# Kernel tuning notes

Measured on AMD Instinct MI355X. Metric: run time of the kernel, lower is better.

The kernel has to match this reference:

```python
import jax, jax.numpy as jnp
import numpy as np

C, N, E = 16, 10000, 40000
OP_DIM, LAY_DIM = 4, 4
NODE_FEAT, CFG_FEAT = 140, 18
GRAPH_IN, GRAPH_OUT, HID = 256, 256, 256
HIDDEN_CH = [256, 256, 256]
N_CONVS = len(HIDDEN_CH) + 1  # 4


def setup_inputs() -> dict:
    key = jax.random.key(0)
    ks = iter(jax.random.split(key, 32))
    inp = {}
    inp['x_node_cfg'] = jax.random.randint(next(ks), (C, N, CFG_FEAT), 0, 8)
    inp['x_feat'] = jax.random.normal(next(ks), (N, NODE_FEAT), dtype=jnp.float32)
    inp['x_op'] = jax.random.randint(next(ks), (N,), 0, 120)
    inp['edge_index'] = jax.random.randint(next(ks), (2, E), 0, N)
    s = 0.05
    inp['emb_op'] = jax.random.normal(next(ks), (120, OP_DIM), dtype=jnp.float32)
    inp['emb_layout'] = jax.random.normal(next(ks), (8, LAY_DIM), dtype=jnp.float32)
    in_dim = OP_DIM + NODE_FEAT + CFG_FEAT * LAY_DIM  # 216
    inp['lin_w'] = jax.random.normal(next(ks), (in_dim, GRAPH_IN), dtype=jnp.float32) * s
    inp['lin_b'] = jnp.zeros((GRAPH_IN,), dtype=jnp.float32)
    # all conv dims are 256 -> stack
    inp['conv_wl'] = jax.random.normal(next(ks), (N_CONVS, GRAPH_IN, GRAPH_IN), dtype=jnp.float32) * s
    inp['conv_bl'] = jnp.zeros((N_CONVS, GRAPH_IN), dtype=jnp.float32)
    inp['conv_wr'] = jax.random.normal(next(ks), (N_CONVS, GRAPH_IN, GRAPH_IN), dtype=jnp.float32) * s
    inp['w1'] = jax.random.normal(next(ks), (GRAPH_OUT, HID), dtype=jnp.float32) * s
    inp['b1'] = jnp.zeros((HID,), dtype=jnp.float32)
    inp['w2'] = jax.random.normal(next(ks), (HID, HID), dtype=jnp.float32) * s
    inp['b2'] = jnp.zeros((HID,), dtype=jnp.float32)
    inp['w3'] = jax.random.normal(next(ks), (HID, 1), dtype=jnp.float32) * s
    inp['b3'] = jnp.zeros((1,), dtype=jnp.float32)
    return inp


def reference(x_node_cfg, x_feat, x_op, edge_index, emb_op, emb_layout,
              lin_w, lin_b, conv_wl, conv_bl, conv_wr, w1, b1, w2, b2, w3, b3):
    c, n = x_node_cfg.shape[0], x_node_cfg.shape[1]
    # feature build: layout-config embedding [C,N,18*4], repeated node feat, op embedding
    cfg = emb_layout[x_node_cfg].reshape(c, n, -1)                    # [C,N,72]
    feat = jnp.broadcast_to(x_feat[None], (c, n, x_feat.shape[1]))    # [C,N,140]
    op = jnp.broadcast_to(emb_op[x_op][None], (c, n, emb_op.shape[1]))# [C,N,4]
    x = jnp.concatenate([feat, cfg, op], axis=2)                      # [C,N,216]
    x = x @ lin_w + lin_b                                             # [C,N,256]

    src, dst = edge_index[0], edge_index[1]
    deg = jnp.zeros((n,), x.dtype).at[dst].add(1.0)
    inv_deg = 1.0 / jnp.maximum(deg, 1.0)                             # scatter-mean denom
    for i in range(conv_wl.shape[0]):
        # SAGEConv: out = lin_l(mean_{j in N(i)} x_j) + lin_r(x_i)
        agg = jnp.zeros_like(x).at[:, dst, :].add(x[:, src, :])
        agg = agg * inv_deg[None, :, None]
        x = jax.nn.relu(agg @ conv_wl[i] + conv_bl[i] + x @ conv_wr[i])

    g = x.mean(axis=1)                                                # [C,256] mean pool
    h = jax.nn.relu(g @ w1 + b1)
    h = jax.nn.relu(h @ w2 + b2)
    out = h @ w3 + b3                                                 # [C,1]
    return out.reshape(-1)
```

## Files before the change

### kernel.cpp

```cpp
#include <hip/hip_runtime.h>

#define N_NODES 10000
#define N_CFG   16
#define N_EDGES 40000
#define UW      512

typedef __attribute__((ext_vector_type(8))) short bf16x8;
typedef __attribute__((ext_vector_type(4))) float floatx4;

__device__ __forceinline__ unsigned short f2bf(float f) {
    union { float f; unsigned int u; } v; v.f = f;
    unsigned int r = (v.u + 0x7fffu + ((v.u >> 16) & 1u)) >> 16;
    return (unsigned short)r;
}
__device__ __forceinline__ float bf2f(unsigned short h) {
    union { unsigned int u; float f; } v; v.u = ((unsigned int)h) << 16;
    return v.f;
}
__device__ __forceinline__ void add8(float* acc, uint4 v) {
    acc[0] += bf2f(v.x & 0xffff); acc[1] += bf2f(v.x >> 16);
    acc[2] += bf2f(v.y & 0xffff); acc[3] += bf2f(v.y >> 16);
    acc[4] += bf2f(v.z & 0xffff); acc[5] += bf2f(v.z >> 16);
    acc[6] += bf2f(v.w & 0xffff); acc[7] += bf2f(v.w >> 16);
}

__device__ __forceinline__ void gl_lds16(const unsigned short* g, unsigned short* l) {
    __builtin_amdgcn_global_load_lds(
        (const __attribute__((address_space(1))) unsigned int*)g,
        (__attribute__((address_space(3))) unsigned int*)l, 16, 0, 0);
}


__global__ __launch_bounds__(256) void k_table(const float* __restrict__ emb_layout,
                                               const float* __restrict__ lin_w,
                                               unsigned short* __restrict__ T) {
    int b = blockIdx.x;
    int j = b >> 3, v = b & 7;
    int d = threadIdx.x;
    float s = 0.f;
#pragma unroll
    for (int t = 0; t < 4; ++t)
        s = fmaf(emb_layout[v * 4 + t], lin_w[(140 + 4 * j + t) * 256 + d], s);
    T[b * 256 + d] = f2bf(s);
}

__global__ __launch_bounds__(256) void k_base(const float* __restrict__ x_feat,
                                              const int* __restrict__ x_op,
                                              const float* __restrict__ emb_op,
                                              const float* __restrict__ lin_w,
                                              const float* __restrict__ lin_b,
                                              unsigned short* __restrict__ base) {
    __shared__ float xf[20][144];
    const int tid = threadIdx.x;
    const int n0 = blockIdx.x * 20;
    for (int j = tid; j < 20 * 140; j += 256)
        xf[j / 140][j % 140] = x_feat[(n0 + j / 140) * 140 + (j % 140)];
    if (tid < 80) {
        int i = tid >> 2, t = tid & 3;
        xf[i][140 + t] = emb_op[x_op[n0 + i] * 4 + t];
    }
    __syncthreads();
    const int d = tid;
    float acc[20];
#pragma unroll
    for (int i = 0; i < 20; ++i) acc[i] = 0.f;
    for (int k = 0; k < 140; ++k) {
        float w = lin_w[k * 256 + d];
#pragma unroll
        for (int i = 0; i < 20; ++i) acc[i] = fmaf(xf[i][k], w, acc[i]);
    }
#pragma unroll
    for (int t = 0; t < 4; ++t) {
        float w = lin_w[(212 + t) * 256 + d];
#pragma unroll
        for (int i = 0; i < 20; ++i) acc[i] = fmaf(xf[i][140 + t], w, acc[i]);
    }
    float bb = lin_b[d];
#pragma unroll
    for (int i = 0; i < 20; ++i)
        base[(n0 + i) * 256 + d] = f2bf(acc[i] + bb);
}

template <int CH>
__global__ __launch_bounds__(256) void k_x0(const unsigned short* __restrict__ base,
                                            const unsigned short* __restrict__ T,
                                            const int* __restrict__ cfg,
                                            unsigned short* __restrict__ U,
                                            int cc) {
    __shared__ int idx[8][18];
    const int tid = threadIdx.x;
    const int n0 = blockIdx.x * 8;
    const int cy = blockIdx.y;
    const int cg = cc * CH + cy;
    if (tid < 144) {
        int nl = tid / 18, j = tid % 18;
        idx[nl][j] = cfg[((size_t)cg * N_NODES + n0 + nl) * 18 + j];
    }
    __syncthreads();
    const int nl = tid >> 5;
    const int colg = (tid & 31) * 8;
    const int n = n0 + nl;
    float acc[8];
    uint4 bv = *(const uint4*)(base + n * 256 + colg);
    acc[0] = bf2f(bv.x & 0xffff); acc[1] = bf2f(bv.x >> 16);
    acc[2] = bf2f(bv.y & 0xffff); acc[3] = bf2f(bv.y >> 16);
    acc[4] = bf2f(bv.z & 0xffff); acc[5] = bf2f(bv.z >> 16);
    acc[6] = bf2f(bv.w & 0xffff); acc[7] = bf2f(bv.w >> 16);
#pragma unroll
    for (int j = 0; j < 18; ++j) {
        uint4 tv = *(const uint4*)(T + (j * 8 + idx[nl][j]) * 256 + colg);
        add8(acc, tv);
    }
    uint4 o;
    o.x = (unsigned int)f2bf(acc[0]) | ((unsigned int)f2bf(acc[1]) << 16);
    o.y = (unsigned int)f2bf(acc[2]) | ((unsigned int)f2bf(acc[3]) << 16);
    o.z = (unsigned int)f2bf(acc[4]) | ((unsigned int)f2bf(acc[5]) << 16);
    o.w = (unsigned int)f2bf(acc[6]) | ((unsigned int)f2bf(acc[7]) << 16);
    *(uint4*)(U + ((size_t)cy * N_NODES + n) * UW + 256 + colg) = o;
}


__global__ void k_deg(const int* __restrict__ ei, int* __restrict__ deg) {
    int e = blockIdx.x * 256 + threadIdx.x;
    if (e < N_EDGES) atomicAdd(&deg[ei[N_EDGES + e]], 1);
}

__global__ __launch_bounds__(256) void k_scan(const int* __restrict__ deg,
                                              int* __restrict__ coff,
                                              float* __restrict__ invd) {
    __shared__ int part[257];
    int t = threadIdx.x;
    const int CHk = 40;
    int start = t * CHk;
    int s = 0;
    for (int i = 0; i < CHk; ++i) {
        int idx = start + i;
        if (idx < N_NODES) s += deg[idx];
    }
    part[t + 1] = s;
    if (t == 0) part[0] = 0;
    __syncthreads();
    if (t == 0)
        for (int i = 1; i <= 256; ++i) part[i] += part[i - 1];
    __syncthreads();
    int run = part[t];
    for (int i = 0; i < CHk; ++i) {
        int idx = start + i;
        if (idx < N_NODES) {
            int d = deg[idx];
            coff[idx] = run; run += d;
            invd[idx] = 1.0f / fmaxf((float)d, 1.0f);
        }
    }
    if (t == 0) coff[N_NODES] = part[256];
}

__global__ void k_fill(const int* __restrict__ ei, const int* __restrict__ coff,
                       int* __restrict__ cur, int* __restrict__ csrc) {
    int e = blockIdx.x * 256 + threadIdx.x;
    if (e < N_EDGES) {
        int d = ei[N_EDGES + e];
        int s = ei[e];
        int pos = atomicAdd(&cur[d], 1);
        csrc[coff[d] + pos] = s;
    }
}

__global__ void k_wsplit(const float* __restrict__ wl, const float* __restrict__ wr,
                         unsigned short* __restrict__ WT) {
    int t = blockIdx.x * 256 + threadIdx.x;
    int i = t >> 17;
    int r = (t >> 8) & 511;
    int nn = t & 255;
    float w = (r < 256) ? wl[i * 65536 + r * 256 + nn]
                        : wr[i * 65536 + (r - 256) * 256 + nn];
    unsigned short hi = f2bf(w);
    unsigned short lo = f2bf(w - bf2f(hi));
    size_t b = (size_t)i * 262144 + (size_t)nn * 1024;
    WT[b + r] = hi;
    WT[b + 512 + r] = lo;
}


__global__ __launch_bounds__(256) void k_agg(unsigned short* __restrict__ U,
                                             const int* __restrict__ coff,
                                             const int* __restrict__ csrc,
                                             const float* __restrict__ invd) {
    const int wave = threadIdx.x >> 6, lane = threadIdx.x & 63;
    const int n = blockIdx.x * 4 + wave;
    const size_t cbase = (size_t)blockIdx.y * 4 * N_NODES;
    const int e0 = coff[n], e1 = coff[n + 1];
    const int h = lane >> 5;
    const int cg = (lane & 31) * 8;
    float acc[4][8];
#pragma unroll
    for (int cy = 0; cy < 4; ++cy)
#pragma unroll
        for (int j = 0; j < 8; ++j) acc[cy][j] = 0.f;
    for (int e = e0 + h; e < e1; e += 2) {
        int s = csrc[e];
        const unsigned short* p = U + (cbase + s) * UW + 256 + cg;
#pragma unroll
        for (int cy = 0; cy < 4; ++cy) {
            uint4 v = *(const uint4*)(p + (size_t)cy * N_NODES * UW);
            add8(acc[cy], v);
        }
    }
#pragma unroll
    for (int cy = 0; cy < 4; ++cy)
#pragma unroll
        for (int j = 0; j < 8; ++j)
            acc[cy][j] += __shfl_xor(acc[cy][j], 32, 64);
    if (h == 0) {
        float iv = invd[n];
#pragma unroll
        for (int cy = 0; cy < 4; ++cy) {
            uint4 o;
            o.x = (unsigned int)f2bf(acc[cy][0] * iv) |
                  ((unsigned int)f2bf(acc[cy][1] * iv) << 16);
            o.y = (unsigned int)f2bf(acc[cy][2] * iv) |
                  ((unsigned int)f2bf(acc[cy][3] * iv) << 16);
            o.z = (unsigned int)f2bf(acc[cy][4] * iv) |
                  ((unsigned int)f2bf(acc[cy][5] * iv) << 16);
            o.w = (unsigned int)f2bf(acc[cy][6] * iv) |
                  ((unsigned int)f2bf(acc[cy][7] * iv) << 16);
            *(uint4*)(U + (cbase + (size_t)cy * N_NODES + n) * UW + cg) = o;
        }
    }
}


__global__ __launch_bounds__(512) void k_gemm(unsigned short* __restrict__ U,
                                              const unsigned short* __restrict__ WTl,
                                              const float* __restrict__ bias) {
    __shared__ unsigned short Asm[128 * 32];
    __shared__ unsigned short Bh[256 * 32];
    __shared__ unsigned short Bl[256 * 32];
    const int tid = threadIdx.x;
    const int lane = tid & 63;
    const int wave = tid >> 6;
    const int wm = wave >> 2;
    const int wn = wave & 3;
    const size_t r0 = (size_t)blockIdx.x * 128;

    const int srow = tid >> 2;
    const int gc = (tid & 3) ^ ((srow >> 1) & 3);

    const int colg = lane & 15, kg = lane >> 4, quad = lane >> 4;
    int aoff[4], boff[4];
#pragma unroll
    for (int t = 0; t < 4; ++t) {
        int ar = wm * 64 + t * 16 + colg;
        aoff[t] = ar * 32 + ((kg ^ ((ar >> 1) & 3)) << 3);
        int br = wn * 64 + t * 16 + colg;
        boff[t] = br * 32 + ((kg ^ ((br >> 1) & 3)) << 3);
    }

    floatx4 acc[4][4];
#pragma unroll
    for (int i = 0; i < 4; ++i)
#pragma unroll
        for (int j = 0; j < 4; ++j) acc[i][j] = (floatx4){0.f, 0.f, 0.f, 0.f};

    const unsigned short* Arow  = U + (r0 + srow) * UW + gc * 8;
    const unsigned short* Wrow0 = WTl + (size_t)srow * 1024 + gc * 8;
    const unsigned short* Wrow1 = WTl + (size_t)(128 + srow) * 1024 + gc * 8;

    for (int kt = 0; kt < 512; kt += 32) {
        gl_lds16(Arow + kt, Asm + tid * 8);
        gl_lds16(Wrow0 + kt,       Bh + tid * 8);
        gl_lds16(Wrow1 + kt,       Bh + 4096 + tid * 8);
        gl_lds16(Wrow0 + 512 + kt, Bl + tid * 8);
        gl_lds16(Wrow1 + 512 + kt, Bl + 4096 + tid * 8);
        __syncthreads();

        bf16x8 a[4], bh[4], bl[4];
#pragma unroll
        for (int t = 0; t < 4; ++t) a[t] = *(const bf16x8*)(Asm + aoff[t]);
#pragma unroll
        for (int t = 0; t < 4; ++t) {
            bh[t] = *(const bf16x8*)(Bh + boff[t]);
            bl[t] = *(const bf16x8*)(Bl + boff[t]);
        }
#pragma unroll
        for (int ti = 0; ti < 4; ++ti)
#pragma unroll
            for (int tj = 0; tj < 4; ++tj)
                acc[ti][tj] = __builtin_amdgcn_mfma_f32_16x16x32_bf16(
                    a[ti], bh[tj], acc[ti][tj], 0, 0, 0);
#pragma unroll
        for (int ti = 0; ti < 4; ++ti)
#pragma unroll
            for (int tj = 0; tj < 4; ++tj)
                acc[ti][tj] = __builtin_amdgcn_mfma_f32_16x16x32_bf16(
                    a[ti], bl[tj], acc[ti][tj], 0, 0, 0);
        __syncthreads();
    }

#pragma unroll
    for (int tj = 0; tj < 4; ++tj) {
        int nn = wn * 64 + tj * 16 + colg;
        float bv = bias[nn];
#pragma unroll
        for (int ti = 0; ti < 4; ++ti) {
#pragma unroll
            for (int r = 0; r < 4; ++r) {
                size_t mm = r0 + (size_t)(wm * 64 + ti * 16 + quad * 4 + r);
                float y = acc[ti][tj][r] + bv;
                U[mm * UW + 256 + nn] = f2bf(fmaxf(y, 0.f));
            }
        }
    }
}


template <int CH>
__global__ __launch_bounds__(256) void k_pool(const unsigned short* __restrict__ U,
                                              float* __restrict__ g, int cc) {
    int cy = blockIdx.y;
    int d = threadIdx.x;
    size_t row0 = (size_t)cy * N_NODES + blockIdx.x * 250;
    float s = 0.f;
    for (int i = 0; i < 250; ++i)
        s += bf2f(U[(row0 + i) * UW + 256 + d]);
    atomicAdd(&g[(cc * CH + cy) * 256 + d], s);
}

__global__ __launch_bounds__(256) void k_head(const float* __restrict__ g,
                                              const float* __restrict__ w1,
                                              const float* __restrict__ b1,
                                              const float* __restrict__ w2,
                                              const float* __restrict__ b2,
                                              const float* __restrict__ w3,
                                              const float* __restrict__ b3,
                                              float* __restrict__ out) {
    __shared__ float ha[256];
    __shared__ float hb[256];
    __shared__ float red[4];
    int c = blockIdx.x;
    int d = threadIdx.x;
    ha[d] = g[c * 256 + d] / 10000.0f;
    __syncthreads();
    float s = b1[d];
#pragma unroll 4
    for (int k = 0; k < 256; ++k)
        s = fmaf(ha[k], w1[k * 256 + d], s);
    hb[d] = fmaxf(s, 0.f);
    __syncthreads();
    s = b2[d];
#pragma unroll 4
    for (int k = 0; k < 256; ++k)
        s = fmaf(hb[k], w2[k * 256 + d], s);
    ha[d] = fmaxf(s, 0.f);
    __syncthreads();
    float p = ha[d] * w3[d];
#pragma unroll
    for (int off = 32; off > 0; off >>= 1)
        p += __shfl_down(p, off, 64);
    if ((d & 63) == 0) red[d >> 6] = p;
    __syncthreads();
    if (d == 0)
        out[c] = red[0] + red[1] + red[2] + red[3] + b3[0];
}

__global__ void k_wsfail(float* __restrict__ out, float v) {
    out[threadIdx.x] = v;
}


extern "C" void kernel_launch(void* const* d_in, const int* in_sizes, int n_in,
                              void* d_out, int out_size, void* d_ws, size_t ws_size,
                              hipStream_t stream) {
    const int*   x_node_cfg = (const int*)  d_in[0];
    const float* x_feat     = (const float*)d_in[1];
    const int*   x_op       = (const int*)  d_in[2];
    const int*   edge_index = (const int*)  d_in[3];
    const float* emb_op     = (const float*)d_in[4];
    const float* emb_layout = (const float*)d_in[5];
    const float* lin_w      = (const float*)d_in[6];
    const float* lin_b      = (const float*)d_in[7];
    const float* conv_wl    = (const float*)d_in[8];
    const float* conv_bl    = (const float*)d_in[9];
    const float* conv_wr    = (const float*)d_in[10];
    const float* w1         = (const float*)d_in[11];
    const float* b1         = (const float*)d_in[12];
    const float* w2         = (const float*)d_in[13];
    const float* b2         = (const float*)d_in[14];
    const float* w3         = (const float*)d_in[15];
    const float* b3         = (const float*)d_in[16];
    float* out = (float*)d_out;

    const size_t NEED8  = (size_t)8  * N_NODES * UW * 2 + 7627268;
    const size_t NEED16 = (size_t)16 * N_NODES * UW * 2 + 7627268;
    const int CH = (ws_size >= NEED16) ? 16 : 8;

    unsigned short* U    = (unsigned short*)d_ws;
    unsigned short* base = U + (size_t)CH * N_NODES * UW;
    unsigned short* T    = base + 2560000;
    unsigned short* WT   = T + 36864;
    float* invd = (float*)(WT + 1048576);
    float* g    = invd + 10000;
    int* deg  = (int*)(g + 4096);
    int* coff = deg + 10000;
    int* cur  = coff + 10001;
    int* csrc = cur + 10000;

    if (ws_size < NEED8) {
        k_wsfail<<<1, 16, 0, stream>>>(out, (float)ws_size * 1e-9f);
        return;
    }

    hipMemsetAsync(deg, 0, N_NODES * sizeof(int), stream);
    hipMemsetAsync(cur, 0, N_NODES * sizeof(int), stream);
    hipMemsetAsync(g, 0, 4096 * sizeof(float), stream);

    k_table<<<144, 256, 0, stream>>>(emb_layout, lin_w, T);
    k_base<<<500, 256, 0, stream>>>(x_feat, x_op, emb_op, lin_w, lin_b, base);
    k_deg<<<(N_EDGES + 255) / 256, 256, 0, stream>>>(edge_index, deg);
    k_scan<<<1, 256, 0, stream>>>(deg, coff, invd);
    k_fill<<<(N_EDGES + 255) / 256, 256, 0, stream>>>(edge_index, coff, cur, csrc);
    k_wsplit<<<2048, 256, 0, stream>>>(conv_wl, conv_wr, WT);

    if (CH == 16) {
        k_x0<16><<<dim3(1250, 16), 256, 0, stream>>>(base, T, x_node_cfg, U, 0);
        for (int i = 0; i < 4; ++i) {
            k_agg<<<dim3(2500, 4), 256, 0, stream>>>(U, coff, csrc, invd);
            k_gemm<<<16 * N_NODES / 128, 512, 0, stream>>>(U, WT + i * 262144,
                                                           conv_bl + i * 256);
        }
        k_pool<16><<<dim3(40, 16), 256, 0, stream>>>(U, g, 0);
    } else {
        for (int cc = 0; cc < 2; ++cc) {
            k_x0<8><<<dim3(1250, 8), 256, 0, stream>>>(base, T, x_node_cfg, U, cc);
            for (int i = 0; i < 4; ++i) {
                k_agg<<<dim3(2500, 2), 256, 0, stream>>>(U, coff, csrc, invd);
                k_gemm<<<8 * N_NODES / 128, 512, 0, stream>>>(U, WT + i * 262144,
                                                              conv_bl + i * 256);
            }
            k_pool<8><<<dim3(40, 8), 256, 0, stream>>>(U, g, cc);
        }
    }

    k_head<<<16, 256, 0, stream>>>(g, w1, b1, w2, b2, w3, b3, out);
}
```

Baseline: 860.1 us.

## Fuse mean-pool into final SAGE GEMM epilogue and halve configs per agg block

Removes the separate pooling kernel by accumulating per-config column sums of the last layer's ReLU output inside the GEMM epilogue. The sums are reduced across quads with shuffles and added to the pooled buffer with atomics, handling the case where a 64-row wave tile straddles two configs. Separately, the aggregation kernel now handles 2 configs per block instead of 4, doubling the grid size. This trades lower register pressure and more parallelism against re-reading the CSR indices more often, and adds atomic traffic to the last GEMM.

```diff
diff --git a/kernel.cpp b/kernel.cpp
--- a/kernel.cpp
+++ b/kernel.cpp
@@ -188,33 +188,32 @@
                                              const float* __restrict__ invd) {
     const int wave = threadIdx.x >> 6, lane = threadIdx.x & 63;
     const int n = blockIdx.x * 4 + wave;
-    const size_t cbase = (size_t)blockIdx.y * 4 * N_NODES;
+    const size_t cbase = (size_t)blockIdx.y * 2 * N_NODES;
     const int e0 = coff[n], e1 = coff[n + 1];
     const int h = lane >> 5;
     const int cg = (lane & 31) * 8;
-    float acc[4][8];
-#pragma unroll
-    for (int cy = 0; cy < 4; ++cy)
+    float acc[2][8];
+#pragma unroll
+    for (int cy = 0; cy < 2; ++cy)
 #pragma unroll
         for (int j = 0; j < 8; ++j) acc[cy][j] = 0.f;
     for (int e = e0 + h; e < e1; e += 2) {
         int s = csrc[e];
         const unsigned short* p = U + (cbase + s) * UW + 256 + cg;
-#pragma unroll
-        for (int cy = 0; cy < 4; ++cy) {
-            uint4 v = *(const uint4*)(p + (size_t)cy * N_NODES * UW);
-            add8(acc[cy], v);
-        }
-    }
-#pragma unroll
-    for (int cy = 0; cy < 4; ++cy)
+        uint4 v0 = *(const uint4*)(p);
+        uint4 v1 = *(const uint4*)(p + (size_t)N_NODES * UW);
+        add8(acc[0], v0);
+        add8(acc[1], v1);
+    }
+#pragma unroll
+    for (int cy = 0; cy < 2; ++cy)
 #pragma unroll
         for (int j = 0; j < 8; ++j)
             acc[cy][j] += __shfl_xor(acc[cy][j], 32, 64);
     if (h == 0) {
         float iv = invd[n];
 #pragma unroll
-        for (int cy = 0; cy < 4; ++cy) {
+        for (int cy = 0; cy < 2; ++cy) {
             uint4 o;
             o.x = (unsigned int)f2bf(acc[cy][0] * iv) |
                   ((unsigned int)f2bf(acc[cy][1] * iv) << 16);
@@ -232,7 +231,8 @@
 
 __global__ __launch_bounds__(512) void k_gemm(unsigned short* __restrict__ U,
                                               const unsigned short* __restrict__ WTl,
-                                              const float* __restrict__ bias) {
+                                              const float* __restrict__ bias,
+                                              int do_pool, float* __restrict__ grow) {
     __shared__ unsigned short Asm[128 * 32];
     __shared__ unsigned short Bh[256 * 32];
     __shared__ unsigned short Bl[256 * 32];
@@ -297,34 +297,41 @@
         __syncthreads();
     }
 
+    const int baseRow = (int)r0 + wm * 64;
+    const int cfgA = baseRow / N_NODES;
 #pragma unroll
     for (int tj = 0; tj < 4; ++tj) {
         int nn = wn * 64 + tj * 16 + colg;
         float bv = bias[nn];
+        float psumA = 0.f, psumB = 0.f;
 #pragma unroll
         for (int ti = 0; ti < 4; ++ti) {
 #pragma unroll
             for (int r = 0; r < 4; ++r) {
-                size_t mm = r0 + (size_t)(wm * 64 + ti * 16 + quad * 4 + r);
+                int row = baseRow + ti * 16 + quad * 4 + r;
                 float y = acc[ti][tj][r] + bv;
-                U[mm * UW + 256 + nn] = f2bf(fmaxf(y, 0.f));
+                unsigned short yb = f2bf(fmaxf(y, 0.f));
+                U[(size_t)row * UW + 256 + nn] = yb;
+                if (do_pool) {
+                    float yv = bf2f(yb);
+                    if (row / N_NODES == cfgA) psumA += yv; else psumB += yv;
+                }
             }
         }
-    }
-}
-
-
-template <int CH>
-__global__ __launch_bounds__(256) void k_pool(const unsigned short* __restrict__ U,
-                                              float* __restrict__ g, int cc) {
-    int cy = blockIdx.y;
-    int d = threadIdx.x;
-    size_t row0 = (size_t)cy * N_NODES + blockIdx.x * 250;
-    float s = 0.f;
-    for (int i = 0; i < 250; ++i)
-        s += bf2f(U[(row0 + i) * UW + 256 + d]);
-    atomicAdd(&g[(cc * CH + cy) * 256 + d], s);
-}
+        if (do_pool) {
+            psumA += __shfl_xor(psumA, 16, 64);
+            psumA += __shfl_xor(psumA, 32, 64);
+            psumB += __shfl_xor(psumB, 16, 64);
+            psumB += __shfl_xor(psumB, 32, 64);
+            if (quad == 0) {
+                atomicAdd(&grow[cfgA * 256 + nn], psumA);
+                if (psumB != 0.f)
+                    atomicAdd(&grow[(cfgA + 1) * 256 + nn], psumB);
+            }
+        }
+    }
+}
+
 
 __global__ __launch_bounds__(256) void k_head(const float* __restrict__ g,
                                               const float* __restrict__ w1,
@@ -424,20 +431,19 @@
     if (CH == 16) {
         k_x0<16><<<dim3(1250, 16), 256, 0, stream>>>(base, T, x_node_cfg, U, 0);
         for (int i = 0; i < 4; ++i) {
-            k_agg<<<dim3(2500, 4), 256, 0, stream>>>(U, coff, csrc, invd);
-            k_gemm<<<16 * N_NODES / 128, 512, 0, stream>>>(U, WT + i * 262144,
-                                                           conv_bl + i * 256);
-        }
-        k_pool<16><<<dim3(40, 16), 256, 0, stream>>>(U, g, 0);
+            k_agg<<<dim3(2500, 8), 256, 0, stream>>>(U, coff, csrc, invd);
+            k_gemm<<<16 * N_NODES / 128, 512, 0, stream>>>(
+                U, WT + i * 262144, conv_bl + i * 256, (i == 3) ? 1 : 0, g);
+        }
     } else {
         for (int cc = 0; cc < 2; ++cc) {
             k_x0<8><<<dim3(1250, 8), 256, 0, stream>>>(base, T, x_node_cfg, U, cc);
             for (int i = 0; i < 4; ++i) {
-                k_agg<<<dim3(2500, 2), 256, 0, stream>>>(U, coff, csrc, invd);
-                k_gemm<<<8 * N_NODES / 128, 512, 0, stream>>>(U, WT + i * 262144,
-                                                              conv_bl + i * 256);
+                k_agg<<<dim3(2500, 4), 256, 0, stream>>>(U, coff, csrc, invd);
+                k_gemm<<<8 * N_NODES / 128, 512, 0, stream>>>(
+                    U, WT + i * 262144, conv_bl + i * 256, (i == 3) ? 1 : 0,
+                    g + cc * 8 * 256);
             }
-            k_pool<8><<<dim3(40, 8), 256, 0, stream>>>(U, g, cc);
         }
     }
 
```

New measurement: 871.2 us. No clear change (+1.3%).
